# Kernel tuning notes

Hardware: AMD Instinct MI355X
Metric: run time of the kernel (lower is better)

## Reference

```python
import jax, jax.numpy as jnp
import numpy as np

N_NODES = 100000
N_EDGES = 1600000
IN_FEAT = 64
OUT_FEAT = 64


def setup_inputs() -> dict:
    key = jax.random.key(0)
    k_feat, k_src, k_dst, k_tw, k_tb, k_pw, k_pb = jax.random.split(key, 7)
    bound = 1.0 / np.sqrt(IN_FEAT)
    return {
        "feat": jax.random.normal(k_feat, (N_NODES, IN_FEAT), dtype=jnp.float32),
        "src": jax.random.randint(k_src, (N_EDGES,), 0, N_NODES, dtype=jnp.int32),
        "dst": jax.random.randint(k_dst, (N_EDGES,), 0, N_NODES, dtype=jnp.int32),
        "theta_w": jax.random.uniform(k_tw, (OUT_FEAT, IN_FEAT), jnp.float32, -bound, bound),
        "theta_b": jax.random.uniform(k_tb, (OUT_FEAT,), jnp.float32, -bound, bound),
        "phi_w": jax.random.uniform(k_pw, (OUT_FEAT, IN_FEAT), jnp.float32, -bound, bound),
        "phi_b": jax.random.uniform(k_pb, (OUT_FEAT,), jnp.float32, -bound, bound),
    }


def reference(feat, src, dst, theta_w, theta_b, phi_w, phi_b):
    # Two dense projections: h_theta = theta(feat), h_phi = phi(feat)
    h_theta = feat @ theta_w.T + theta_b          # [N, out_feat]
    h_phi = feat @ phi_w.T + phi_b                # [N, out_feat]
    diff = h_phi - h_theta                        # dstdata['x']
    # u_add_v: per-edge message e = h_theta[src] + (h_phi - h_theta)[dst]
    e = h_theta[src] + diff[dst]                  # [E, out_feat]
    # fn.max('e', 'x'): segment max over destination nodes
    out = jax.ops.segment_max(e, dst, num_segments=N_NODES)  # [N, out_feat]
    # DGL fills zero-in-degree destinations with 0 (segment_max yields -inf)
    return jnp.where(jnp.isfinite(out), out, jnp.float32(0))
```

## Files before the change

kernel.cpp:

```cpp
#include <hip/hip_runtime.h>
#include <hip/hip_bf16.h>
#include <hip/hip_fp16.h>

#define F 64
#define BSH 7
#define NBMAX 1024
#define XG 8
#define SUBCAP 512
#define CHUNK 4096
#define EPT 8
#define BCAP 4096
#define WPAD 72
#define SPAD 136

typedef __bf16 bf16x8 __attribute__((ext_vector_type(8)));
typedef float  f32x4  __attribute__((ext_vector_type(4)));
typedef unsigned int uint4v __attribute__((ext_vector_type(4)));

__device__ inline unsigned pkmax(unsigned a, unsigned b) {
    unsigned d;
    asm volatile("v_pk_max_f16 %0, %1, %2" : "=v"(d) : "v"(a), "v"(b));
    return d;
}
__device__ inline uint4v pkmax4(uint4v a, uint4v b) {
    uint4v r;
    r.x = pkmax(a.x, b.x); r.y = pkmax(a.y, b.y);
    r.z = pkmax(a.z, b.z); r.w = pkmax(a.w, b.w);
    return r;
}
__device__ inline float half_lo(unsigned u) {
    union { unsigned short s; _Float16 h; } c; c.s = (unsigned short)(u & 0xFFFF);
    return (float)c.h;
}
__device__ inline float half_hi(unsigned u) {
    union { unsigned short s; _Float16 h; } c; c.s = (unsigned short)(u >> 16);
    return (float)c.h;
}
__device__ inline void casmax(unsigned* a, unsigned val) {
    unsigned old = *a;
    while (true) {
        unsigned nw = pkmax(old, val);
        if (nw == old) break;
        unsigned prev = atomicCAS(a, old, nw);
        if (prev == old) break;
        old = prev;
    }
}

union FusedSh {
    struct {
        union {
            __bf16  w2t[128 * WPAD];
            _Float16 stage[128 * SPAD];
        } u;
        float bias[128];
    } p;
    struct {
        int cur[NBMAX]; int gb[NBMAX]; int lbeg[NBMAX];
        int fs[512];
        unsigned sw[CHUNK];
        unsigned short sb[CHUNK];
    } b;
};

__global__ __launch_bounds__(512) void fused_proj_bin(
    const float* __restrict__ feat,
    const float* __restrict__ theta_w, const float* __restrict__ theta_b,
    const float* __restrict__ phi_w,  const float* __restrict__ phi_b,
    _Float16* __restrict__ h16, _Float16* __restrict__ d16,
    const int* __restrict__ src, const int* __restrict__ dst,
    int* __restrict__ bcnt, unsigned* __restrict__ packed,
    int n_nodes, int n_edges, int nb, int bin_blocks)
{
    __shared__ FusedSh sh;
    const int t = threadIdx.x;

    if (blockIdx.x < bin_blocks) {
        const int xcdg = blockIdx.x & (XG - 1);
        const int base = blockIdx.x * CHUNK;
        const int cnt = min(CHUNK, n_edges - base);

        for (int i = t; i < NBMAX; i += 512) sh.b.cur[i] = 0;
        __syncthreads();

        unsigned w[EPT];
        int      bk[EPT];
        int      rk[EPT];
        const int k0 = t * EPT;

        if (k0 + EPT <= cnt) {
            #pragma unroll
            for (int j = 0; j < EPT; ++j) {
                int k = k0 + j;
                int s = src[base + k], d = dst[base + k];
                w[j]  = ((unsigned)(d & ((1 << BSH) - 1)) << 17) | (unsigned)s;
                int b = d >> BSH;
                bk[j] = b;
                rk[j] = atomicAdd(&sh.b.cur[b], 1);
            }
        } else {
            #pragma unroll
            for (int j = 0; j < EPT; ++j) {
                int k = k0 + j;
                bk[j] = -1;
                if (k < cnt) {
                    int s = src[base + k], d = dst[base + k];
                    w[j]  = ((unsigned)(d & ((1 << BSH) - 1)) << 17) | (unsigned)s;
                    int b = d >> BSH;
                    bk[j] = b;
                    rk[j] = atomicAdd(&sh.b.cur[b], 1);
                }
            }
        }
        __syncthreads();

        for (int i = t; i < nb; i += 512) {
            int c = sh.b.cur[i];
            sh.b.gb[i] = c ? atomicAdd(&bcnt[xcdg * NBMAX + i], c) : 0;
        }

        int c0 = sh.b.cur[2 * t];
        int c1 = sh.b.cur[2 * t + 1];
        int s2 = c0 + c1;
        sh.b.fs[t] = s2;
        __syncthreads();
        for (int off = 1; off < 512; off <<= 1) {
            int x = (t >= off) ? sh.b.fs[t - off] : 0;
            __syncthreads();
            sh.b.fs[t] += x;
            __syncthreads();
        }
        {
            int exc = sh.b.fs[t] - s2;
            sh.b.lbeg[2 * t]     = exc;
            sh.b.lbeg[2 * t + 1] = exc + c0;
        }
        __syncthreads();

        #pragma unroll
        for (int j = 0; j < EPT; ++j) {
            if (bk[j] >= 0) {
                int slot = sh.b.lbeg[bk[j]] + rk[j];
                sh.b.sw[slot] = w[j];
                sh.b.sb[slot] = (unsigned short)bk[j];
            }
        }
        __syncthreads();

        #pragma unroll
        for (int r = 0; r < EPT; ++r) {
            int p = r * 512 + t;
            if (p < cnt) {
                int b = sh.b.sb[p];
                int pos = sh.b.gb[b] + (p - sh.b.lbeg[b]);
                if (pos < SUBCAP)
                    packed[((size_t)b * XG + xcdg) * SUBCAP + pos] = sh.b.sw[p];
            }
        }
    } else {
        const int pb = blockIdx.x - bin_blocks;
        const int chunkbase = pb * 128;

        for (int i = t; i < 128 * 64; i += 512) {
            int n = i >> 6, k = i & 63;
            float v = (n < 64) ? theta_w[n * 64 + k]
                               : phi_w[(n - 64) * 64 + k] - theta_w[(n - 64) * 64 + k];
            sh.p.u.w2t[n * WPAD + k] = (__bf16)v;
        }
        if (t < 128) {
            int n = t;
            sh.p.bias[n] = (n < 64) ? theta_b[n] : (phi_b[n - 64] - theta_b[n - 64]);
        }
        __syncthreads();

        const int lane = t & 63;
        const int wv   = t >> 6;
        const int m    = lane & 15;
        const int q    = lane >> 4;

        const int rowbase = chunkbase + wv * 16;
        int arow = rowbase + m;
        int rs = arow < n_nodes ? arow : 0;

        bf16x8 a0, a1;
        {
            const float* p0 = feat + (size_t)rs * 64 + q * 8;
            #pragma unroll
            for (int j = 0; j < 8; ++j) a0[j] = (__bf16)p0[j];
            #pragma unroll
            for (int j = 0; j < 8; ++j) a1[j] = (__bf16)p0[32 + j];
        }

        f32x4 acc[8];
        #pragma unroll
        for (int c = 0; c < 8; ++c) acc[c] = (f32x4){0.f, 0.f, 0.f, 0.f};

        #pragma unroll
        for (int c = 0; c < 8; ++c) {
            const __bf16* wp = &sh.p.u.w2t[(c * 16 + m) * WPAD + q * 8];
            bf16x8 b0 = *(const bf16x8*)wp;
            bf16x8 b1 = *(const bf16x8*)(wp + 32);
            acc[c] = __builtin_amdgcn_mfma_f32_16x16x32_bf16(a0, b0, acc[c], 0, 0, 0);
            acc[c] = __builtin_amdgcn_mfma_f32_16x16x32_bf16(a1, b1, acc[c], 0, 0, 0);
        }

        __syncthreads();

        const int rloc = wv * 16 + q * 4;
        #pragma unroll
        for (int c = 0; c < 8; ++c) {
            float bb = sh.p.bias[c * 16 + m];
            #pragma unroll
            for (int r = 0; r < 4; ++r)
                sh.p.u.stage[(rloc + r) * SPAD + c * 16 + m] =
                    (_Float16)(acc[c][r] + bb);
        }
        __syncthreads();

        #pragma unroll
        for (int p2 = 0; p2 < 2; ++p2) {
            int idx = p2 * 512 + t;
            int row = idx >> 3, c8 = idx & 7;
            int grow = chunkbase + row;
            if (grow < n_nodes) {
                uint4v hv = *(const uint4v*)&sh.p.u.stage[row * SPAD + c8 * 8];
                uint4v dv = *(const uint4v*)&sh.p.u.stage[row * SPAD + 64 + c8 * 8];
                *(uint4v*)(h16 + (size_t)grow * F + c8 * 8) = hv;
                *(uint4v*)(d16 + (size_t)grow * F + c8 * 8) = dv;
            }
        }
    }
}

__global__ __launch_bounds__(256) void sort_reduce(
    const unsigned* __restrict__ packed, const int* __restrict__ bcnt,
    const _Float16* __restrict__ h16, const _Float16* __restrict__ d16,
    float* __restrict__ out, int n_nodes)
{
    __shared__ unsigned ew[BCAP];
    __shared__ unsigned mx[128 * 32];
    __shared__ int fcnt[128];
    __shared__ int fbg[129];
    __shared__ int fs[256];
    __shared__ int scnt[XG];

    const int b = blockIdx.x, t = threadIdx.x;
    const unsigned NEGI = 0xFC00FC00u;

    #pragma unroll
    for (int i = 0; i < 16; ++i) mx[i * 256 + t] = NEGI;
    if (t < 128) fcnt[t] = 0;
    if (t < XG)  scnt[t] = min(bcnt[t * NBMAX + b], SUBCAP);
    __syncthreads();

    unsigned w[16];
    int      rk[16];
    #pragma unroll
    for (int j = 0; j < 16; ++j) {
        int seg = j >> 1;
        int k   = (j & 1) * 256 + t;
        rk[j] = -1;
        if (k < scnt[seg]) {
            unsigned wrd = packed[((size_t)b * XG + seg) * SUBCAP + k];
            w[j]  = wrd;
            rk[j] = atomicAdd(&fcnt[wrd >> 17], 1);
        }
    }
    __syncthreads();

    int cnt = 0;
    #pragma unroll
    for (int s = 0; s < XG; ++s) cnt += scnt[s];

    int v = (t < 128) ? fcnt[t] : 0;
    fs[t] = v;
    __syncthreads();
    for (int off = 1; off < 128; off <<= 1) {
        int x = (t >= off) ? fs[t - off] : 0;
        __syncthreads();
        fs[t] += x;
        __syncthreads();
    }
    if (t < 128) fbg[t] = fs[t] - v;
    if (t == 0)  fbg[128] = cnt;
    __syncthreads();

    #pragma unroll
    for (int j = 0; j < 16; ++j) {
        if (rk[j] >= 0) {
            unsigned wrd = w[j];
            ew[fbg[wrd >> 17] + rk[j]] = wrd & 0x1FFFFu;
        }
    }
    __syncthreads();

    const int g  = t >> 3;
    const int f8 = t & 7;
    {
        int L0 = (cnt + 31) >> 5;
        int L  = ((L0 + 3) & ~7) | 4;
        int s  = g * L; if (s > cnt) s = cnt;
        int e  = s + L; if (e > cnt) e = cnt;

        if (s < e) {
            int lo = 0, hi = 128;
            while (lo + 1 < hi) {
                int mid = (lo + hi) >> 1;
                if (fbg[mid] <= s) lo = mid; else hi = mid;
            }
            int node = lo;
            int nend = fbg[node + 1];

            uint4v acc = (uint4v){NEGI, NEGI, NEGI, NEGI};
            int p = s;
            for (; p + 4 <= e; p += 4) {
                uint4v sv = *(const uint4v*)&ew[p];
                uint4v v0 = *(const uint4v*)(h16 + (size_t)sv.x * F + f8 * 8);
                uint4v v1 = *(const uint4v*)(h16 + (size_t)sv.y * F + f8 * 8);
                uint4v v2 = *(const uint4v*)(h16 + (size_t)sv.z * F + f8 * 8);
                uint4v v3 = *(const uint4v*)(h16 + (size_t)sv.w * F + f8 * 8);
                while (p >= nend) {
                    unsigned* m0 = &mx[node * 32 + f8 * 4];
                    casmax(m0 + 0, acc.x); casmax(m0 + 1, acc.y);
                    casmax(m0 + 2, acc.z); casmax(m0 + 3, acc.w);
                    acc = (uint4v){NEGI, NEGI, NEGI, NEGI};
                    ++node; nend = fbg[node + 1];
                }
                acc = pkmax4(acc, v0);
                while (p + 1 >= nend) {
                    unsigned* m0 = &mx[node * 32 + f8 * 4];
                    casmax(m0 + 0, acc.x); casmax(m0 + 1, acc.y);
                    casmax(m0 + 2, acc.z); casmax(m0 + 3, acc.w);
                    acc = (uint4v){NEGI, NEGI, NEGI, NEGI};
                    ++node; nend = fbg[node + 1];
                }
                acc = pkmax4(acc, v1);
                while (p + 2 >= nend) {
                    unsigned* m0 = &mx[node * 32 + f8 * 4];
                    casmax(m0 + 0, acc.x); casmax(m0 + 1, acc.y);
                    casmax(m0 + 2, acc.z); casmax(m0 + 3, acc.w);
                    acc = (uint4v){NEGI, NEGI, NEGI, NEGI};
                    ++node; nend = fbg[node + 1];
                }
                acc = pkmax4(acc, v2);
                while (p + 3 >= nend) {
                    unsigned* m0 = &mx[node * 32 + f8 * 4];
                    casmax(m0 + 0, acc.x); casmax(m0 + 1, acc.y);
                    casmax(m0 + 2, acc.z); casmax(m0 + 3, acc.w);
                    acc = (uint4v){NEGI, NEGI, NEGI, NEGI};
                    ++node; nend = fbg[node + 1];
                }
                acc = pkmax4(acc, v3);
            }
            for (; p < e; ++p) {
                unsigned srcn = ew[p];
                uint4v v0 = *(const uint4v*)(h16 + (size_t)srcn * F + f8 * 8);
                while (p >= nend) {
                    unsigned* m0 = &mx[node * 32 + f8 * 4];
                    casmax(m0 + 0, acc.x); casmax(m0 + 1, acc.y);
                    casmax(m0 + 2, acc.z); casmax(m0 + 3, acc.w);
                    acc = (uint4v){NEGI, NEGI, NEGI, NEGI};
                    ++node; nend = fbg[node + 1];
                }
                acc = pkmax4(acc, v0);
            }
            unsigned* m0 = &mx[node * 32 + f8 * 4];
            casmax(m0 + 0, acc.x); casmax(m0 + 1, acc.y);
            casmax(m0 + 2, acc.z); casmax(m0 + 3, acc.w);
        }
    }
    __syncthreads();

    const int ln0 = t >> 3;
    #pragma unroll
    for (int pass = 0; pass < 4; ++pass) {
        int ln = ln0 + pass * 32;
        int node = (b << BSH) + ln;
        if (node < n_nodes) {
            size_t o = (size_t)node * F + f8 * 8;
            f32x4 r0, r1;
            if (fcnt[ln] > 0) {
                uint4v A  = *(const uint4v*)&mx[ln * 32 + f8 * 4];
                uint4v dv = __builtin_nontemporal_load((const uint4v*)(d16 + o));
                r0[0] = half_lo(dv.x) + half_lo(A.x);
                r0[1] = half_hi(dv.x) + half_hi(A.x);
                r0[2] = half_lo(dv.y) + half_lo(A.y);
                r0[3] = half_hi(dv.y) + half_hi(A.y);
                r1[0] = half_lo(dv.z) + half_lo(A.z);
                r1[1] = half_hi(dv.z) + half_hi(A.z);
                r1[2] = half_lo(dv.w) + half_lo(A.w);
                r1[3] = half_hi(dv.w) + half_hi(A.w);
            } else {
                r0 = (f32x4){0.f, 0.f, 0.f, 0.f};
                r1 = (f32x4){0.f, 0.f, 0.f, 0.f};
            }
            __builtin_nontemporal_store(r0, (f32x4*)(out + o));
            __builtin_nontemporal_store(r1, (f32x4*)(out + o + 4));
        }
    }
}

extern "C" void kernel_launch(void* const* d_in, const int* in_sizes, int n_in,
                              void* d_out, int out_size, void* d_ws, size_t ws_size,
                              hipStream_t stream) {
    const float* feat    = (const float*)d_in[0];
    const int*   src     = (const int*)d_in[1];
    const int*   dst     = (const int*)d_in[2];
    const float* theta_w = (const float*)d_in[3];
    const float* theta_b = (const float*)d_in[4];
    const float* phi_w   = (const float*)d_in[5];
    const float* phi_b   = (const float*)d_in[6];
    float* out = (float*)d_out;

    const int n_nodes = in_sizes[0] / F;
    const int n_edges = in_sizes[1];
    const int nb      = (n_nodes + (1 << BSH) - 1) >> BSH;

    _Float16* h16    = (_Float16*)d_ws;
    _Float16* d16    = h16 + (size_t)n_nodes * F;
    unsigned* packed = (unsigned*)(d16 + (size_t)n_nodes * F);
    int*      bcnt   = (int*)(packed + (size_t)nb * XG * SUBCAP);

    hipMemsetAsync(bcnt, 0, XG * NBMAX * sizeof(int), stream);

    const int bin_blocks  = (n_edges + CHUNK - 1) / CHUNK;
    const int proj_blocks = (n_nodes + 127) / 128;
    fused_proj_bin<<<bin_blocks + proj_blocks, 512, 0, stream>>>(
        feat, theta_w, theta_b, phi_w, phi_b, h16, d16,
        src, dst, bcnt, packed, n_nodes, n_edges, nb, bin_blocks);

    sort_reduce<<<nb, 256, 0, stream>>>(packed, bcnt, h16, d16, out, n_nodes);
}
```

Baseline: 142.3 us.

## Double sort_reduce block size and replace shared-memory scan with wave shuffle scan

Launches sort_reduce with 512 threads per block instead of 256, so each thread loads one packed edge per segment and there are 64 edge groups instead of 32. The 128-bin exclusive prefix sum now runs in a single wavefront with shuffle-up, replacing a shared-memory scan that needed many barriers. More threads give more parallelism per block, but also more LDS atomic contention and fewer registers per thread. The scan relies on a 64-lane wavefront.

Result: slower. 145.9 us (+2.5%).

```diff
diff --git a/kernel.cpp b/kernel.cpp
--- a/kernel.cpp
+++ b/kernel.cpp
@@ -232,7 +232,7 @@
     }
 }
 
-__global__ __launch_bounds__(256) void sort_reduce(
+__global__ __launch_bounds__(512) void sort_reduce(
     const unsigned* __restrict__ packed, const int* __restrict__ bcnt,
     const _Float16* __restrict__ h16, const _Float16* __restrict__ d16,
     float* __restrict__ out, int n_nodes)
@@ -241,27 +241,24 @@
     __shared__ unsigned mx[128 * 32];
     __shared__ int fcnt[128];
     __shared__ int fbg[129];
-    __shared__ int fs[256];
     __shared__ int scnt[XG];
 
     const int b = blockIdx.x, t = threadIdx.x;
     const unsigned NEGI = 0xFC00FC00u;
 
     #pragma unroll
-    for (int i = 0; i < 16; ++i) mx[i * 256 + t] = NEGI;
+    for (int i = 0; i < 8; ++i) mx[i * 512 + t] = NEGI;
     if (t < 128) fcnt[t] = 0;
     if (t < XG)  scnt[t] = min(bcnt[t * NBMAX + b], SUBCAP);
     __syncthreads();
 
-    unsigned w[16];
-    int      rk[16];
+    unsigned w[XG];
+    int      rk[XG];
     #pragma unroll
-    for (int j = 0; j < 16; ++j) {
-        int seg = j >> 1;
-        int k   = (j & 1) * 256 + t;
+    for (int j = 0; j < XG; ++j) {
         rk[j] = -1;
-        if (k < scnt[seg]) {
-            unsigned wrd = packed[((size_t)b * XG + seg) * SUBCAP + k];
+        if (t < scnt[j]) {
+            unsigned wrd = packed[((size_t)b * XG + j) * SUBCAP + t];
             w[j]  = wrd;
             rk[j] = atomicAdd(&fcnt[wrd >> 17], 1);
         }
@@ -272,21 +269,22 @@
     #pragma unroll
     for (int s = 0; s < XG; ++s) cnt += scnt[s];
 
-    int v = (t < 128) ? fcnt[t] : 0;
-    fs[t] = v;
+    if (t < 64) {
+        int a = fcnt[2 * t], c = fcnt[2 * t + 1];
+        int s = a + c;
+        #pragma unroll
+        for (int d = 1; d < 64; d <<= 1) {
+            int x = __shfl_up(s, d);
+            if (t >= d) s += x;
+        }
+        fbg[2 * t]     = s - c - a;
+        fbg[2 * t + 1] = s - c;
+        if (t == 63) fbg[128] = s;
+    }
     __syncthreads();
-    for (int off = 1; off < 128; off <<= 1) {
-        int x = (t >= off) ? fs[t - off] : 0;
-        __syncthreads();
-        fs[t] += x;
-        __syncthreads();
-    }
-    if (t < 128) fbg[t] = fs[t] - v;
-    if (t == 0)  fbg[128] = cnt;
-    __syncthreads();
 
     #pragma unroll
-    for (int j = 0; j < 16; ++j) {
+    for (int j = 0; j < XG; ++j) {
         if (rk[j] >= 0) {
             unsigned wrd = w[j];
             ew[fbg[wrd >> 17] + rk[j]] = wrd & 0x1FFFFu;
@@ -297,7 +295,7 @@
     const int g  = t >> 3;
     const int f8 = t & 7;
     {
-        int L0 = (cnt + 31) >> 5;
+        int L0 = (cnt + 63) >> 6;
         int L  = ((L0 + 3) & ~7) | 4;
         int s  = g * L; if (s > cnt) s = cnt;
         int e  = s + L; if (e > cnt) e = cnt;
@@ -373,8 +371,8 @@
 
     const int ln0 = t >> 3;
     #pragma unroll
-    for (int pass = 0; pass < 4; ++pass) {
-        int ln = ln0 + pass * 32;
+    for (int pass = 0; pass < 2; ++pass) {
+        int ln = ln0 + pass * 64;
         int node = (b << BSH) + ln;
         if (node < n_nodes) {
             size_t o = (size_t)node * F + f8 * 8;
@@ -429,5 +427,5 @@
         feat, theta_w, theta_b, phi_w, phi_b, h16, d16,
         src, dst, bcnt, packed, n_nodes, n_edges, nb, bin_blocks);
 
-    sort_reduce<<<nb, 256, 0, stream>>>(packed, bcnt, h16, d16, out, n_nodes);
-}
+    sort_reduce<<<nb, 512, 0, stream>>>(packed, bcnt, h16, d16, out, n_nodes);
+}
```
